# Optimization experiments

Hardware: AMD Instinct MI355X
Metric: run time of the kernel (lower is better)

The kernel has to match this reference:

```python
import jax, jax.numpy as jnp
import numpy as np

DIM = 512
NUM_HEADS = 8
POS_DIM = 2
K_CLUSTERS = 256
M_PTS = 256


def setup_inputs() -> dict:
    key = jax.random.key(0)
    ks = jax.random.split(key, 9)
    pos = jax.random.uniform(ks[0], (K_CLUSTERS, M_PTS, POS_DIM), dtype=jnp.float32)
    feat = jax.random.normal(ks[1], (K_CLUSTERS, M_PTS, DIM), dtype=jnp.float32)
    mask = jax.random.randint(ks[2], (K_CLUSTERS, M_PTS, 1), 0, 2, dtype=jnp.int32)
    s = 0.02
    qkv_w = jax.random.normal(ks[3], (DIM, 3 * DIM), dtype=jnp.float32) * s
    qkv_b = jnp.zeros((3 * DIM,), dtype=jnp.float32)
    pos_w = jax.random.normal(ks[4], (POS_DIM, NUM_HEADS), dtype=jnp.float32) * s
    pos_b = jnp.zeros((NUM_HEADS,), dtype=jnp.float32)
    proj_w = jax.random.normal(ks[5], (DIM, DIM), dtype=jnp.float32) * s
    proj_b = jnp.zeros((DIM,), dtype=jnp.float32)
    return {"pos": pos, "feat": feat, "qkv_w": qkv_w, "qkv_b": qkv_b,
            "pos_w": pos_w, "pos_b": pos_b, "proj_w": proj_w, "proj_b": proj_b,
            "mask": mask}


def reference(pos, feat, qkv_w, qkv_b, pos_w, pos_b, proj_w, proj_b, mask):
    k_, m, c = feat.shape
    H = pos_w.shape[1]
    hd = c // H
    scale = hd ** -0.5

    # qkv projection -> (3, k, H, m, hd)
    qkv = (feat @ qkv_w + qkv_b).reshape(k_, m, 3, H, hd).transpose(2, 0, 3, 1, 4)
    q, k, v = qkv[0], qkv[1], qkv[2]

    attn = jnp.einsum('khid,khjd->khij', q * scale, k)  # k,H,m,m

    # normalize each coordinate by its global max over all clusters/points
    pos_n = pos / jnp.max(pos, axis=(0, 1), keepdims=True)
    # rel_pos[k,a,b,d] = pos[k,b,d] - pos[k,a,d]
    rel_pos = pos_n[:, None, :, :] - pos_n[:, :, None, :]  # k,m,m,d
    pos_bias = rel_pos @ pos_w + pos_b                      # k,m,m,H
    attn = attn + pos_bias.transpose(0, 3, 1, 2)            # k,H,m,m

    # mask: k,m,1 -> additive bias over key dim
    maskf = mask[:, :, 0].astype(attn.dtype)                # k,m
    attn = attn + ((1.0 - maskf) * -100.0)[:, None, None, :]

    attn = jax.nn.softmax(attn, axis=-1)
    x = jnp.einsum('khij,khjd->khid', attn, v)              # k,H,m,hd
    x = x.transpose(0, 2, 1, 3).reshape(k_, m, c)
    x = x @ proj_w + proj_b
    return x
```

## Files before the change

kernel.cpp:

```cpp
#include <hip/hip_runtime.h>
#include <stdint.h>

typedef short bf16x8 __attribute__((ext_vector_type(8)));
typedef float f32x4 __attribute__((ext_vector_type(4)));
typedef unsigned short u16x4 __attribute__((ext_vector_type(4)));
typedef unsigned short ushort_t;

__device__ __forceinline__ float bf2f(unsigned short u) {
    union { unsigned int i; float f; } v; v.i = ((unsigned int)u) << 16; return v.f;
}
__device__ __forceinline__ unsigned short f2bf(float f) {
    union { float f; unsigned int i; } v; v.f = f;
    unsigned int r = (v.i + 0x7FFFu + ((v.i >> 16) & 1u)) >> 16;
    return (unsigned short)r;
}

__device__ __forceinline__ void gload_lds16(const void* g, void* l) {
    __builtin_amdgcn_global_load_lds(
        (const __attribute__((address_space(1))) void*)g,
        (__attribute__((address_space(3))) void*)l, 16, 0, 0);
}

template <bool F32> struct LD;
template <> struct LD<false> {
    static __device__ __forceinline__ float s(const void* p, size_t i) {
        return bf2f(((const ushort_t*)p)[i]);
    }
    static __device__ __forceinline__ bf16x8 v8(const void* p, size_t i) {
        return *reinterpret_cast<const bf16x8*>((const ushort_t*)p + i);
    }
};
template <> struct LD<true> {
    static __device__ __forceinline__ float s(const void* p, size_t i) {
        return ((const float*)p)[i];
    }
    static __device__ __forceinline__ bf16x8 v8(const void* p, size_t i) {
        const float* f = (const float*)p + i;
        float4 a = *reinterpret_cast<const float4*>(f);
        float4 b = *reinterpret_cast<const float4*>(f + 4);
        bf16x8 r;
        r[0] = (short)f2bf(a.x); r[1] = (short)f2bf(a.y);
        r[2] = (short)f2bf(a.z); r[3] = (short)f2bf(a.w);
        r[4] = (short)f2bf(b.x); r[5] = (short)f2bf(b.y);
        r[6] = (short)f2bf(b.z); r[7] = (short)f2bf(b.w);
        return r;
    }
};

__global__ __launch_bounds__(64) void kprobe(const ushort_t* __restrict__ pos, int* __restrict__ dt) {
    float v = bf2f(pos[2 * threadIdx.x]);
    bool sane = (v >= 0.0f) && (v <= 1.0f);
    unsigned long long b = __ballot(sane);
    if (threadIdx.x == 0) dt[0] = (b == ~0ULL) ? 1 : 0;
}

template <bool F32>
static __device__ __forceinline__ void kpos_body(const void* pos, int* pmax, float* s0, float* s1) {
    int p = blockIdx.x * 256 + threadIdx.x;
    s0[threadIdx.x] = LD<F32>::s(pos, 2 * (size_t)p);
    s1[threadIdx.x] = LD<F32>::s(pos, 2 * (size_t)p + 1);
    __syncthreads();
    for (int off = 128; off > 0; off >>= 1) {
        if (threadIdx.x < (unsigned)off) {
            s0[threadIdx.x] = fmaxf(s0[threadIdx.x], s0[threadIdx.x + off]);
            s1[threadIdx.x] = fmaxf(s1[threadIdx.x], s1[threadIdx.x + off]);
        }
        __syncthreads();
    }
    if (threadIdx.x == 0) {
        atomicMax(&pmax[0], __float_as_int(s0[0]));
        atomicMax(&pmax[1], __float_as_int(s1[0]));
    }
}
__global__ __launch_bounds__(256) void kpos_max(const int* __restrict__ dt, const void* __restrict__ pos,
                                                int* __restrict__ pmax) {
    __shared__ float s0[256], s1[256];
    if (dt[0]) kpos_body<false>(pos, pmax, s0, s1);
    else       kpos_body<true>(pos, pmax, s0, s1);
}

template <bool F32>
static __device__ __forceinline__ void ktb_body(const void* pos, const void* pos_w, const int* mask,
                                                const int* pmax, float* tb) {
    int p = blockIdx.x * 256 + threadIdx.x;
    float inv0 = 1.0f / __int_as_float(pmax[0]);
    float inv1 = 1.0f / __int_as_float(pmax[1]);
    float x0 = LD<F32>::s(pos, 2 * (size_t)p) * inv0;
    float x1 = LD<F32>::s(pos, 2 * (size_t)p + 1) * inv1;
    float mterm = mask[p] ? 0.0f : -100.0f;
#pragma unroll
    for (int h = 0; h < 8; h++)
        tb[p * 8 + h] = x0 * LD<F32>::s(pos_w, h) + x1 * LD<F32>::s(pos_w, 8 + h) + mterm;
}
__global__ __launch_bounds__(256) void ktb(const int* __restrict__ dt, const void* __restrict__ pos,
                                           const void* __restrict__ pos_w, const int* __restrict__ mask,
                                           const int* __restrict__ pmax, float* __restrict__ tb) {
    if (dt[0]) ktb_body<false>(pos, pos_w, mask, pmax, tb);
    else       ktb_body<true>(pos, pos_w, mask, pmax, tb);
}

__global__ __launch_bounds__(256) void kbias(const int* __restrict__ dt, const void* __restrict__ qkv_b,
                                             const void* __restrict__ proj_b,
                                             float* __restrict__ qb, float* __restrict__ pb) {
    int i = blockIdx.x * 256 + threadIdx.x;
    if (dt[0]) {
        if (i < 1536) qb[i] = bf2f(((const ushort_t*)qkv_b)[i]);
        if (i < 512)  pb[i] = bf2f(((const ushort_t*)proj_b)[i]);
    } else {
        if (i < 1536) qb[i] = ((const float*)qkv_b)[i];
        if (i < 512)  pb[i] = ((const float*)proj_b)[i];
    }
}

template <bool F32>
static __device__ __forceinline__ void kfeat_body(const void* feat, ushort_t* featb) {
    for (size_t t = (size_t)blockIdx.x * 256 + threadIdx.x; t < 4194304; t += (size_t)gridDim.x * 256) {
        *reinterpret_cast<bf16x8*>(featb + t * 8) = LD<F32>::v8(feat, t * 8);
    }
}
__global__ __launch_bounds__(256) void kfeat(const int* __restrict__ dt, const void* __restrict__ feat,
                                             ushort_t* __restrict__ featb) {
    if (dt[0]) kfeat_body<false>(feat, featb);
    else       kfeat_body<true>(feat, featb);
}

template <bool F32>
static __device__ __forceinline__ void ktrans_body(const void* src, ushort_t* dst, int R, int C,
                                                   ushort_t* tile ) {
    int nbc = C >> 6;
    int rb = (blockIdx.x / nbc) << 6;
    int cb = (blockIdx.x % nbc) << 6;
    for (int i = threadIdx.x; i < 4096; i += 256) {
        int r = i >> 6, c = i & 63;
        tile[r * 65 + c] = f2bf(LD<F32>::s(src, (size_t)(rb + r) * C + cb + c));
    }
    __syncthreads();
    for (int i = threadIdx.x; i < 4096; i += 256) {
        int rr = i & 63, cc = i >> 6;
        dst[(size_t)(cb + cc) * R + rb + rr] = tile[rr * 65 + cc];
    }
}
__global__ __launch_bounds__(256) void ktrans(const int* __restrict__ dt, const void* __restrict__ src,
                                              ushort_t* __restrict__ dst, int R, int C) {
    __shared__ ushort_t tile[64 * 65];
    if (dt[0]) ktrans_body<false>(src, dst, R, C, tile);
    else       ktrans_body<true>(src, dst, R, C, tile);
}

template <bool F32>
static __device__ __forceinline__ void kattn_body(const void* feat, const ushort_t* qkv_wt,
                                                  const float* qb, const float* tb, ushort_t* xout,
                                                  ushort_t* sQ, ushort_t* sK, ushort_t* sVt,
                                                  ushort_t* sP, float* stb) {
    const int tid = threadIdx.x;
    const int lane = tid & 63;
    const int wave = tid >> 6;
    const int quad = lane >> 4;
    const int l15 = lane & 15;

    const int bx = blockIdx.x;
    const int xcd = bx & 7;
    const int jj = bx >> 3;
    const int rr = jj >> 5;
    const int ss = jj & 31;
    const int kc = xcd * 32 + rr * 4 + (ss >> 3);
    const int h = ss & 7;

    if (tid < 256) stb[tid] = tb[(size_t)(kc * 256 + tid) * 8 + h];

    ushort_t* sW = sP;
    char* ldsW = (char*)sW;

    const int t1 = wave * 64 + lane;
    const int t2 = 512 + t1;
    const int lc1 = t1 >> 2, ch1 = t1 & 3;
    const int lc2 = t2 >> 2, ch2 = t2 & 3;
    const ushort_t* g1 = qkv_wt + (size_t)((lc1 >> 6) * 512 + h * 64 + (lc1 & 63)) * 512 + ch1 * 8;
    const ushort_t* g2 = qkv_wt + (size_t)((lc2 >> 6) * 512 + h * 64 + (lc2 & 63)) * 512 + ch2 * 8;

    const int wrow = (wave >> 1) * 64;
    const int wcol = (wave & 1) * 96;
    const int fcol = quad * 8;

    f32x4 acc[4][6];
#pragma unroll
    for (int rt = 0; rt < 4; rt++)
#pragma unroll
        for (int ct = 0; ct < 6; ct++) {
            f32x4 z = {0.0f, 0.0f, 0.0f, 0.0f};
            acc[rt][ct] = z;
        }

    const size_t fbase = (size_t)(kc * 256) * 512;

    gload_lds16(g1, ldsW + wave * 1024);
    if (wave < 4) gload_lds16(g2, ldsW + 8192 + wave * 1024);
    __syncthreads();

#pragma unroll 2
    for (int c = 0; c < 16; c++) {
        const int cb = (c & 1) * 6144;
        const int nbB = ((c + 1) & 1) * 12288;
        if (c < 15) {
            gload_lds16(g1 + (c + 1) * 32, ldsW + nbB + wave * 1024);
            if (wave < 4) gload_lds16(g2 + (c + 1) * 32, ldsW + nbB + 8192 + wave * 1024);
        }
        bf16x8 af[4];
#pragma unroll
        for (int rt = 0; rt < 4; rt++)
            af[rt] = LD<F32>::v8(feat, fbase + (size_t)(wrow + rt * 16 + l15) * 512 + c * 32 + fcol);
        bf16x8 bw[6];
#pragma unroll
        for (int ct = 0; ct < 6; ct++)
            bw[ct] = *reinterpret_cast<const bf16x8*>(sW + cb + (wcol + ct * 16 + l15) * 32 + fcol);
#pragma unroll
        for (int ct = 0; ct < 6; ct++)
#pragma unroll
            for (int rt = 0; rt < 4; rt++)
                acc[rt][ct] = __builtin_amdgcn_mfma_f32_16x16x32_bf16(af[rt], bw[ct], acc[rt][ct], 0, 0, 0);
        __syncthreads();
    }

#pragma unroll
    for (int ct = 0; ct < 6; ct++) {
        const int lcb = wcol + ct * 16;
        const int mat = lcb >> 6;
        const int col = (lcb & 63) + l15;
        const float bias = qb[mat * 512 + h * 64 + col];
#pragma unroll
        for (int rt = 0; rt < 4; rt++) {
            const int m0 = wrow + rt * 16 + quad * 4;
            if (mat == 0) {
#pragma unroll
                for (int r = 0; r < 4; r++)
                    sQ[(m0 + r) * 72 + col] = f2bf((acc[rt][ct][r] + bias) * 0.125f);
            } else if (mat == 1) {
#pragma unroll
                for (int r = 0; r < 4; r++)
                    sK[(m0 + r) * 72 + col] = f2bf(acc[rt][ct][r] + bias);
            } else {
                u16x4 vp;
#pragma unroll
                for (int r = 0; r < 4; r++) vp[r] = f2bf(acc[rt][ct][r] + bias);
                *reinterpret_cast<u16x4*>(&sVt[col * 264 + m0]) = vp;
            }
        }
    }
    __syncthreads();

    bf16x8 aQ[2][2];
#pragma unroll
    for (int rt = 0; rt < 2; rt++)
#pragma unroll
        for (int s = 0; s < 2; s++)
            aQ[rt][s] = *reinterpret_cast<const bf16x8*>(
                &sQ[(wave * 32 + rt * 16 + l15) * 72 + s * 32 + quad * 8]);

    f32x4 accO[2][4];
    float rs[2][4];
#pragma unroll
    for (int rt = 0; rt < 2; rt++)
#pragma unroll
        for (int ct = 0; ct < 4; ct++) {
            f32x4 z = {0.0f, 0.0f, 0.0f, 0.0f};
            accO[rt][ct] = z;
            rs[rt][ct] = 0.0f;
        }

    ushort_t* sPw = sP + wave * (32 * 72);

    for (int jb = 0; jb < 4; jb++) {
        int kb = jb * 64;
        bf16x8 bK[4][2];
#pragma unroll
        for (int ctk = 0; ctk < 4; ctk++)
#pragma unroll
            for (int s = 0; s < 2; s++)
                bK[ctk][s] = *reinterpret_cast<const bf16x8*>(
                    &sK[(kb + ctk * 16 + l15) * 72 + s * 32 + quad * 8]);

#pragma unroll
        for (int ctk = 0; ctk < 4; ctk++) {
            float tcol = stb[kb + ctk * 16 + l15];
#pragma unroll
            for (int rt = 0; rt < 2; rt++) {
                f32x4 sa = {0.0f, 0.0f, 0.0f, 0.0f};
                sa = __builtin_amdgcn_mfma_f32_16x16x32_bf16(aQ[rt][0], bK[ctk][0], sa, 0, 0, 0);
                sa = __builtin_amdgcn_mfma_f32_16x16x32_bf16(aQ[rt][1], bK[ctk][1], sa, 0, 0, 0);
                int rl0 = rt * 16 + quad * 4;
#pragma unroll
                for (int r = 0; r < 4; r++) {
                    float pexp = __expf(sa[r] + tcol);
                    rs[rt][r] += pexp;
                    sPw[(rl0 + r) * 72 + ctk * 16 + l15] = f2bf(pexp);
                }
            }
        }

#pragma unroll
        for (int s = 0; s < 2; s++) {
            bf16x8 aP[2];
#pragma unroll
            for (int rt = 0; rt < 2; rt++)
                aP[rt] = *reinterpret_cast<const bf16x8*>(
                    &sPw[(rt * 16 + l15) * 72 + s * 32 + quad * 8]);
#pragma unroll
            for (int ct = 0; ct < 4; ct++) {
                bf16x8 bV = *reinterpret_cast<const bf16x8*>(
                    &sVt[(ct * 16 + l15) * 264 + kb + s * 32 + quad * 8]);
#pragma unroll
                for (int rt = 0; rt < 2; rt++)
                    accO[rt][ct] =
                        __builtin_amdgcn_mfma_f32_16x16x32_bf16(aP[rt], bV, accO[rt][ct], 0, 0, 0);
            }
        }
    }

    float inv_[2][4];
#pragma unroll
    for (int rt = 0; rt < 2; rt++)
#pragma unroll
        for (int r = 0; r < 4; r++) {
            float v = rs[rt][r];
            v += __shfl_xor(v, 1, 64);
            v += __shfl_xor(v, 2, 64);
            v += __shfl_xor(v, 4, 64);
            v += __shfl_xor(v, 8, 64);
            inv_[rt][r] = 1.0f / v;
        }

#pragma unroll
    for (int rt = 0; rt < 2; rt++)
#pragma unroll
        for (int ct = 0; ct < 4; ct++)
#pragma unroll
            for (int r = 0; r < 4; r++) {
                int m = wave * 32 + rt * 16 + quad * 4 + r;
                xout[((size_t)(kc * 256 + m)) * 512 + h * 64 + ct * 16 + l15] =
                    f2bf(accO[rt][ct][r] * inv_[rt][r]);
            }
}
__global__ __launch_bounds__(512, 2) void kattn_bf(const ushort_t* __restrict__ featb,
                                                   const ushort_t* __restrict__ qkv_wt,
                                                   const float* __restrict__ qb,
                                                   const float* __restrict__ tb, ushort_t* __restrict__ xout) {
    __shared__ ushort_t sQ[256 * 72];
    __shared__ ushort_t sK[256 * 72];
    __shared__ ushort_t sVt[64 * 264];
    __shared__ ushort_t sP[8 * 32 * 72];
    __shared__ float stb[256];
    kattn_body<false>(featb, qkv_wt, qb, tb, xout, sQ, sK, sVt, sP, stb);
}
__global__ __launch_bounds__(512, 2) void kattn_dyn(const int* __restrict__ dt, const void* __restrict__ feat,
                                                    const ushort_t* __restrict__ qkv_wt,
                                                    const float* __restrict__ qb,
                                                    const float* __restrict__ tb, ushort_t* __restrict__ xout) {
    __shared__ ushort_t sQ[256 * 72];
    __shared__ ushort_t sK[256 * 72];
    __shared__ ushort_t sVt[64 * 264];
    __shared__ ushort_t sP[8 * 32 * 72];
    __shared__ float stb[256];
    if (dt[0]) kattn_body<false>(feat, qkv_wt, qb, tb, xout, sQ, sK, sVt, sP, stb);
    else       kattn_body<true>(feat, qkv_wt, qb, tb, xout, sQ, sK, sVt, sP, stb);
}

template <bool F32>
static __device__ __forceinline__ void kproj_body(const ushort_t* x, const ushort_t* proj_wt,
                                                  const float* pb, void* out, ushort_t* sW) {
    const int tid = threadIdx.x;
    const int lane = tid & 63;
    const int wave = tid >> 6;
    const int quad = lane >> 4;
    const int l15 = lane & 15;
    const int rowb = (blockIdx.x & 255) * 256 + wave * 64;
    const int colb = (blockIdx.x >> 8) * 128;
    char* ldsW = (char*)sW;

    const int t1 = wave * 64 + lane;
    const int t2 = t1 + 256;
    const ushort_t* g1 = proj_wt + (size_t)(colb + (t1 >> 2)) * 512 + (t1 & 3) * 8;
    const ushort_t* g2 = proj_wt + (size_t)(colb + (t2 >> 2)) * 512 + (t2 & 3) * 8;

    f32x4 acc[4][8];
#pragma unroll
    for (int rt = 0; rt < 4; rt++)
#pragma unroll
        for (int ct = 0; ct < 8; ct++) {
            f32x4 z = {0.0f, 0.0f, 0.0f, 0.0f};
            acc[rt][ct] = z;
        }

    gload_lds16(g1, ldsW + wave * 1024);
    gload_lds16(g2, ldsW + 4096 + wave * 1024);
    __syncthreads();

#pragma unroll 2
    for (int c = 0; c < 16; c++) {
        const int cb = (c & 1) * 4096;
        const int nbB = ((c + 1) & 1) * 8192;
        if (c < 15) {
            gload_lds16(g1 + (c + 1) * 32, ldsW + nbB + wave * 1024);
            gload_lds16(g2 + (c + 1) * 32, ldsW + nbB + 4096 + wave * 1024);
        }
        bf16x8 af[4];
#pragma unroll
        for (int rt = 0; rt < 4; rt++) {
            int m = rowb + rt * 16 + l15;
            af[rt] = *reinterpret_cast<const bf16x8*>(x + (size_t)m * 512 + c * 32 + quad * 8);
        }
        bf16x8 bw[8];
#pragma unroll
        for (int ct = 0; ct < 8; ct++)
            bw[ct] = *reinterpret_cast<const bf16x8*>(sW + cb + (ct * 16 + l15) * 32 + quad * 8);
#pragma unroll
        for (int ct = 0; ct < 8; ct++)
#pragma unroll
            for (int rt = 0; rt < 4; rt++)
                acc[rt][ct] = __builtin_amdgcn_mfma_f32_16x16x32_bf16(af[rt], bw[ct], acc[rt][ct], 0, 0, 0);
        __syncthreads();
    }

#pragma unroll
    for (int ct = 0; ct < 8; ct++) {
        int n = colb + ct * 16 + l15;
        float bias = pb[n];
#pragma unroll
        for (int rt = 0; rt < 4; rt++)
#pragma unroll
            for (int r = 0; r < 4; r++) {
                int m = rowb + rt * 16 + quad * 4 + r;
                float v = acc[rt][ct][r] + bias;
                if (F32) ((float*)out)[(size_t)m * 512 + n] = v;
                else     ((ushort_t*)out)[(size_t)m * 512 + n] = f2bf(v);
            }
    }
}
__global__ __launch_bounds__(256, 2) void kproj(const int* __restrict__ dt, const ushort_t* __restrict__ x,
                                                const ushort_t* __restrict__ proj_wt,
                                                const float* __restrict__ pb, void* __restrict__ out) {
    __shared__ ushort_t sW[2 * 128 * 32];
    if (dt[0]) kproj_body<false>(x, proj_wt, pb, out, sW);
    else       kproj_body<true>(x, proj_wt, pb, out, sW);
}

extern "C" void kernel_launch(void* const* d_in, const int* in_sizes, int n_in,
                              void* d_out, int out_size, void* d_ws, size_t ws_size,
                              hipStream_t stream) {
    (void)in_sizes; (void)n_in; (void)out_size;
    const void* pos    = d_in[0];
    const void* feat   = d_in[1];
    const void* qkv_w  = d_in[2];
    const void* qkv_b  = d_in[3];
    const void* pos_w  = d_in[4];
    const void* proj_w = d_in[6];
    const void* proj_b = d_in[7];
    const int* mask    = (const int*)d_in[8];

    char* ws = (char*)d_ws;
    int* pmax         = (int*)ws;
    int* dtf          = (int*)ws + 2;
    float* qb         = (float*)(ws + 256);
    float* pb         = (float*)(ws + 256 + 6144);
    float* tb         = (float*)(ws + 16384);
    ushort_t* qkv_wt  = (ushort_t*)(ws + 16384 + 2097152);
    ushort_t* proj_wt = qkv_wt + 786432;
    ushort_t* x       = proj_wt + 262144;
    ushort_t* featb   = x + 33554432;
    const size_t NEED = 16384 + 2097152 + 1572864 + 524288 + 67108864 + 67108864;
    const bool big = ws_size >= NEED;

    (void)hipMemsetAsync(ws, 0, 16, stream);
    kprobe<<<1, 64, 0, stream>>>((const ushort_t*)pos, dtf);
    kpos_max<<<256, 256, 0, stream>>>(dtf, pos, pmax);
    ktb<<<256, 256, 0, stream>>>(dtf, pos, pos_w, mask, pmax, tb);
    kbias<<<6, 256, 0, stream>>>(dtf, qkv_b, proj_b, qb, pb);
    ktrans<<<192, 256, 0, stream>>>(dtf, qkv_w, qkv_wt, 512, 1536);
    ktrans<<<64, 256, 0, stream>>>(dtf, proj_w, proj_wt, 512, 512);
    if (big) {
        kfeat<<<2048, 256, 0, stream>>>(dtf, feat, featb);
        kattn_bf<<<2048, 512, 0, stream>>>(featb, qkv_wt, qb, tb, x);
    } else {
        kattn_dyn<<<2048, 512, 0, stream>>>(dtf, feat, qkv_wt, qb, tb, x);
    }
    kproj<<<1024, 256, 0, stream>>>(dtf, x, proj_wt, pb, d_out);
}
```

Measured before the change: 582.1 us.

## Triple-buffer weight tiles with XOR swizzle and prefetch A fragments in GEMMs

Both the QKV stage of the attention kernel and the output projection kernel move from a double-buffered LDS weight pipeline with two __syncthreads per step to a three-stage ring buffer. Each step now needs only one s_barrier, uses manual vmcnt waits, and register-prefetches the next A fragment. LDS weight chunks are XOR-swizzled to cut bank conflicts on the bf16x8 reads. The projection kernel also narrows its column tile to 64 with XCD-aware block mapping and raises occupancy to 3 blocks, doubling the grid. The hand-counted vmcnt values and the single-barrier ring scheme are fragile: if the counts are wrong, it can read stale LDS data.

```diff
diff --git a/kernel.cpp b/kernel.cpp
--- a/kernel.cpp
+++ b/kernel.cpp
@@ -173,14 +173,14 @@
 
     const int t1 = wave * 64 + lane;
     const int t2 = 512 + t1;
-    const int lc1 = t1 >> 2, ch1 = t1 & 3;
-    const int lc2 = t2 >> 2, ch2 = t2 & 3;
+    const int lc1 = t1 >> 2, ch1 = (t1 & 3) ^ ((lc1 >> 1) & 3);
+    const int lc2 = t2 >> 2, ch2 = (t2 & 3) ^ ((lc2 >> 1) & 3);
     const ushort_t* g1 = qkv_wt + (size_t)((lc1 >> 6) * 512 + h * 64 + (lc1 & 63)) * 512 + ch1 * 8;
     const ushort_t* g2 = qkv_wt + (size_t)((lc2 >> 6) * 512 + h * 64 + (lc2 & 63)) * 512 + ch2 * 8;
 
     const int wrow = (wave >> 1) * 64;
     const int wcol = (wave & 1) * 96;
-    const int fcol = quad * 8;
+    const int swz = (l15 >> 1) & 3;
 
     f32x4 acc[4][6];
 #pragma unroll
@@ -192,33 +192,47 @@
         }
 
     const size_t fbase = (size_t)(kc * 256) * 512;
+    bf16x8 af[2][4];
 
     gload_lds16(g1, ldsW + wave * 1024);
     if (wave < 4) gload_lds16(g2, ldsW + 8192 + wave * 1024);
-    __syncthreads();
-
-#pragma unroll 2
+    gload_lds16(g1 + 32, ldsW + 12288 + wave * 1024);
+    if (wave < 4) gload_lds16(g2 + 32, ldsW + 12288 + 8192 + wave * 1024);
+    __builtin_amdgcn_sched_barrier(0);
+#pragma unroll
+    for (int rt = 0; rt < 4; rt++)
+        af[0][rt] = LD<F32>::v8(feat, fbase + (size_t)(wrow + rt * 16 + l15) * 512 + quad * 8);
+    if (F32) asm volatile("s_waitcnt vmcnt(9)" ::: "memory");
+    else     asm volatile("s_waitcnt vmcnt(5)" ::: "memory");
+    __builtin_amdgcn_sched_barrier(0);
+
+#pragma unroll
     for (int c = 0; c < 16; c++) {
-        const int cb = (c & 1) * 6144;
-        const int nbB = ((c + 1) & 1) * 12288;
-        if (c < 15) {
-            gload_lds16(g1 + (c + 1) * 32, ldsW + nbB + wave * 1024);
-            if (wave < 4) gload_lds16(g2 + (c + 1) * 32, ldsW + nbB + 8192 + wave * 1024);
-        }
-        bf16x8 af[4];
-#pragma unroll
-        for (int rt = 0; rt < 4; rt++)
-            af[rt] = LD<F32>::v8(feat, fbase + (size_t)(wrow + rt * 16 + l15) * 512 + c * 32 + fcol);
+        __builtin_amdgcn_s_barrier();
+        __builtin_amdgcn_sched_barrier(0);
+        if (c + 2 < 16) {
+            const int nb = ((c + 2) % 3) * 12288;
+            gload_lds16(g1 + (c + 2) * 32, ldsW + nb + wave * 1024);
+            if (wave < 4) gload_lds16(g2 + (c + 2) * 32, ldsW + nb + 8192 + wave * 1024);
+        }
+        __builtin_amdgcn_sched_barrier(0);
+        if (c + 1 < 16) {
+#pragma unroll
+            for (int rt = 0; rt < 4; rt++)
+                af[(c + 1) & 1][rt] = LD<F32>::v8(
+                    feat, fbase + (size_t)(wrow + rt * 16 + l15) * 512 + (c + 1) * 32 + quad * 8);
+        }
+        const int cbu = (c % 3) * 6144;
         bf16x8 bw[6];
 #pragma unroll
         for (int ct = 0; ct < 6; ct++)
-            bw[ct] = *reinterpret_cast<const bf16x8*>(sW + cb + (wcol + ct * 16 + l15) * 32 + fcol);
+            bw[ct] = *reinterpret_cast<const bf16x8*>(
+                sW + cbu + (wcol + ct * 16 + l15) * 32 + (quad ^ swz) * 8);
 #pragma unroll
         for (int ct = 0; ct < 6; ct++)
 #pragma unroll
             for (int rt = 0; rt < 4; rt++)
-                acc[rt][ct] = __builtin_amdgcn_mfma_f32_16x16x32_bf16(af[rt], bw[ct], acc[rt][ct], 0, 0, 0);
-        __syncthreads();
+                acc[rt][ct] = __builtin_amdgcn_mfma_f32_16x16x32_bf16(af[c & 1][rt], bw[ct], acc[rt][ct], 0, 0, 0);
     }
 
 #pragma unroll
@@ -372,73 +386,83 @@
     const int wave = tid >> 6;
     const int quad = lane >> 4;
     const int l15 = lane & 15;
-    const int rowb = (blockIdx.x & 255) * 256 + wave * 64;
-    const int colb = (blockIdx.x >> 8) * 128;
+    const int bx = blockIdx.x;
+    const int xcd = bx & 7;
+    const int j = bx >> 3;
+    const int rowb = (xcd * 32 + (j >> 3)) * 256;
+    const int colb = (j & 7) * 64;
     char* ldsW = (char*)sW;
 
-    const int t1 = wave * 64 + lane;
-    const int t2 = t1 + 256;
-    const ushort_t* g1 = proj_wt + (size_t)(colb + (t1 >> 2)) * 512 + (t1 & 3) * 8;
-    const ushort_t* g2 = proj_wt + (size_t)(colb + (t2 >> 2)) * 512 + (t2 & 3) * 8;
-
-    f32x4 acc[4][8];
+    const int lc = tid >> 2, ch = (tid & 3) ^ ((lc >> 1) & 3);
+    const ushort_t* g1 = proj_wt + (size_t)(colb + lc) * 512 + ch * 8;
+    const int swz = (l15 >> 1) & 3;
+
+    f32x4 acc[4][4];
 #pragma unroll
     for (int rt = 0; rt < 4; rt++)
 #pragma unroll
-        for (int ct = 0; ct < 8; ct++) {
+        for (int ct = 0; ct < 4; ct++) {
             f32x4 z = {0.0f, 0.0f, 0.0f, 0.0f};
             acc[rt][ct] = z;
         }
 
+    bf16x8 af[2][4];
+
     gload_lds16(g1, ldsW + wave * 1024);
-    gload_lds16(g2, ldsW + 4096 + wave * 1024);
-    __syncthreads();
-
-#pragma unroll 2
+    gload_lds16(g1 + 32, ldsW + 4096 + wave * 1024);
+    __builtin_amdgcn_sched_barrier(0);
+#pragma unroll
+    for (int rt = 0; rt < 4; rt++)
+        af[0][rt] = *reinterpret_cast<const bf16x8*>(
+            x + (size_t)(rowb + wave * 64 + rt * 16 + l15) * 512 + quad * 8);
+    asm volatile("s_waitcnt vmcnt(5)" ::: "memory");
+    __builtin_amdgcn_sched_barrier(0);
+
+#pragma unroll
     for (int c = 0; c < 16; c++) {
-        const int cb = (c & 1) * 4096;
-        const int nbB = ((c + 1) & 1) * 8192;
-        if (c < 15) {
-            gload_lds16(g1 + (c + 1) * 32, ldsW + nbB + wave * 1024);
-            gload_lds16(g2 + (c + 1) * 32, ldsW + nbB + 4096 + wave * 1024);
-        }
-        bf16x8 af[4];
-#pragma unroll
-        for (int rt = 0; rt < 4; rt++) {
-            int m = rowb + rt * 16 + l15;
-            af[rt] = *reinterpret_cast<const bf16x8*>(x + (size_t)m * 512 + c * 32 + quad * 8);
-        }
-        bf16x8 bw[8];
-#pragma unroll
-        for (int ct = 0; ct < 8; ct++)
-            bw[ct] = *reinterpret_cast<const bf16x8*>(sW + cb + (ct * 16 + l15) * 32 + quad * 8);
-#pragma unroll
-        for (int ct = 0; ct < 8; ct++)
+        __builtin_amdgcn_s_barrier();
+        __builtin_amdgcn_sched_barrier(0);
+        if (c + 2 < 16)
+            gload_lds16(g1 + (c + 2) * 32, ldsW + ((c + 2) % 3) * 4096 + wave * 1024);
+        __builtin_amdgcn_sched_barrier(0);
+        if (c + 1 < 16) {
 #pragma unroll
             for (int rt = 0; rt < 4; rt++)
-                acc[rt][ct] = __builtin_amdgcn_mfma_f32_16x16x32_bf16(af[rt], bw[ct], acc[rt][ct], 0, 0, 0);
-        __syncthreads();
-    }
-
-#pragma unroll
-    for (int ct = 0; ct < 8; ct++) {
+                af[(c + 1) & 1][rt] = *reinterpret_cast<const bf16x8*>(
+                    x + (size_t)(rowb + wave * 64 + rt * 16 + l15) * 512 + (c + 1) * 32 + quad * 8);
+        }
+        const int cbu = (c % 3) * 2048;
+        bf16x8 bw[4];
+#pragma unroll
+        for (int ct = 0; ct < 4; ct++)
+            bw[ct] = *reinterpret_cast<const bf16x8*>(
+                sW + cbu + (ct * 16 + l15) * 32 + (quad ^ swz) * 8);
+#pragma unroll
+        for (int ct = 0; ct < 4; ct++)
+#pragma unroll
+            for (int rt = 0; rt < 4; rt++)
+                acc[rt][ct] = __builtin_amdgcn_mfma_f32_16x16x32_bf16(af[c & 1][rt], bw[ct], acc[rt][ct], 0, 0, 0);
+    }
+
+#pragma unroll
+    for (int ct = 0; ct < 4; ct++) {
         int n = colb + ct * 16 + l15;
         float bias = pb[n];
 #pragma unroll
         for (int rt = 0; rt < 4; rt++)
 #pragma unroll
             for (int r = 0; r < 4; r++) {
-                int m = rowb + rt * 16 + quad * 4 + r;
+                int m = rowb + wave * 64 + rt * 16 + quad * 4 + r;
                 float v = acc[rt][ct][r] + bias;
                 if (F32) ((float*)out)[(size_t)m * 512 + n] = v;
                 else     ((ushort_t*)out)[(size_t)m * 512 + n] = f2bf(v);
             }
     }
 }
-__global__ __launch_bounds__(256, 2) void kproj(const int* __restrict__ dt, const ushort_t* __restrict__ x,
+__global__ __launch_bounds__(256, 3) void kproj(const int* __restrict__ dt, const ushort_t* __restrict__ x,
                                                 const ushort_t* __restrict__ proj_wt,
                                                 const float* __restrict__ pb, void* __restrict__ out) {
-    __shared__ ushort_t sW[2 * 128 * 32];
+    __shared__ ushort_t sW[3 * 64 * 32];
     if (dt[0]) kproj_body<false>(x, proj_wt, pb, out, sW);
     else       kproj_body<true>(x, proj_wt, pb, out, sW);
 }
@@ -482,5 +506,5 @@
     } else {
         kattn_dyn<<<2048, 512, 0, stream>>>(dtf, feat, qkv_wt, qb, tb, x);
     }
-    kproj<<<1024, 256, 0, stream>>>(dtf, x, proj_wt, pb, d_out);
-}
+    kproj<<<2048, 256, 0, stream>>>(dtf, x, proj_wt, pb, d_out);
+}
```

Measured after the change: 584.8 us. No clear change (+0.5%).

## Double wave count per block in attention and projection kernels, swizzle LDS weights

Applied to the files above, without the earlier changes.

The attention kernel now launches 1024 threads (16 waves), so each wave owns a 64x48 QKV tile and 16 query rows instead of a 64x96 tile and 32 rows. The projection kernel now uses 512 threads with 64x64 tiles per wave and an XCD-aware block remap. Both stage their weights with an XOR swizzle on the 16-byte chunk index to cut LDS bank conflicts. The aim is more waves in flight and lower register pressure per wave to hide latency. The cost is more redundant global feat/x fragment loads per block and heavier barrier synchronisation.

```diff
diff --git a/kernel.cpp b/kernel.cpp
--- a/kernel.cpp
+++ b/kernel.cpp
@@ -171,50 +171,44 @@
     ushort_t* sW = sP;
     char* ldsW = (char*)sW;
 
-    const int t1 = wave * 64 + lane;
-    const int t2 = 512 + t1;
-    const int lc1 = t1 >> 2, ch1 = t1 & 3;
-    const int lc2 = t2 >> 2, ch2 = t2 & 3;
+    const int lc1 = tid >> 2, ch1 = (tid & 3) ^ ((lc1 >> 1) & 3);
     const ushort_t* g1 = qkv_wt + (size_t)((lc1 >> 6) * 512 + h * 64 + (lc1 & 63)) * 512 + ch1 * 8;
-    const ushort_t* g2 = qkv_wt + (size_t)((lc2 >> 6) * 512 + h * 64 + (lc2 & 63)) * 512 + ch2 * 8;
-
-    const int wrow = (wave >> 1) * 64;
-    const int wcol = (wave & 1) * 96;
-    const int fcol = quad * 8;
-
-    f32x4 acc[4][6];
+    const bool stager = (tid < 768);
+
+    const int wrow = (wave >> 2) * 64;
+    const int wcol = (wave & 3) * 48;
+    const int swz = (l15 >> 1) & 3;
+
+    f32x4 acc[4][3];
 #pragma unroll
     for (int rt = 0; rt < 4; rt++)
 #pragma unroll
-        for (int ct = 0; ct < 6; ct++) {
+        for (int ct = 0; ct < 3; ct++) {
             f32x4 z = {0.0f, 0.0f, 0.0f, 0.0f};
             acc[rt][ct] = z;
         }
 
     const size_t fbase = (size_t)(kc * 256) * 512;
 
-    gload_lds16(g1, ldsW + wave * 1024);
-    if (wave < 4) gload_lds16(g2, ldsW + 8192 + wave * 1024);
+    if (stager) gload_lds16(g1, ldsW + wave * 1024);
     __syncthreads();
 
 #pragma unroll 2
     for (int c = 0; c < 16; c++) {
         const int cb = (c & 1) * 6144;
-        const int nbB = ((c + 1) & 1) * 12288;
-        if (c < 15) {
-            gload_lds16(g1 + (c + 1) * 32, ldsW + nbB + wave * 1024);
-            if (wave < 4) gload_lds16(g2 + (c + 1) * 32, ldsW + nbB + 8192 + wave * 1024);
-        }
+        if (c < 15 && stager)
+            gload_lds16(g1 + (c + 1) * 32, ldsW + ((c + 1) & 1) * 12288 + wave * 1024);
         bf16x8 af[4];
 #pragma unroll
         for (int rt = 0; rt < 4; rt++)
-            af[rt] = LD<F32>::v8(feat, fbase + (size_t)(wrow + rt * 16 + l15) * 512 + c * 32 + fcol);
-        bf16x8 bw[6];
-#pragma unroll
-        for (int ct = 0; ct < 6; ct++)
-            bw[ct] = *reinterpret_cast<const bf16x8*>(sW + cb + (wcol + ct * 16 + l15) * 32 + fcol);
-#pragma unroll
-        for (int ct = 0; ct < 6; ct++)
+            af[rt] = LD<F32>::v8(feat, fbase + (size_t)(wrow + rt * 16 + l15) * 512 + c * 32 + quad * 8);
+        bf16x8 bw[3];
+#pragma unroll
+        for (int ct = 0; ct < 3; ct++)
+            bw[ct] = *reinterpret_cast<const bf16x8*>(
+                sW + cb + (wcol + ct * 16 + l15) * 32 + (quad ^ swz) * 8);
+#pragma unroll
+        for (int ct = 0; ct < 3; ct++)
 #pragma unroll
             for (int rt = 0; rt < 4; rt++)
                 acc[rt][ct] = __builtin_amdgcn_mfma_f32_16x16x32_bf16(af[rt], bw[ct], acc[rt][ct], 0, 0, 0);
@@ -222,7 +216,7 @@
     }
 
 #pragma unroll
-    for (int ct = 0; ct < 6; ct++) {
+    for (int ct = 0; ct < 3; ct++) {
         const int lcb = wcol + ct * 16;
         const int mat = lcb >> 6;
         const int col = (lcb & 63) + l15;
@@ -248,26 +242,22 @@
     }
     __syncthreads();
 
-    bf16x8 aQ[2][2];
-#pragma unroll
-    for (int rt = 0; rt < 2; rt++)
-#pragma unroll
-        for (int s = 0; s < 2; s++)
-            aQ[rt][s] = *reinterpret_cast<const bf16x8*>(
-                &sQ[(wave * 32 + rt * 16 + l15) * 72 + s * 32 + quad * 8]);
-
-    f32x4 accO[2][4];
-    float rs[2][4];
-#pragma unroll
-    for (int rt = 0; rt < 2; rt++)
-#pragma unroll
-        for (int ct = 0; ct < 4; ct++) {
-            f32x4 z = {0.0f, 0.0f, 0.0f, 0.0f};
-            accO[rt][ct] = z;
-            rs[rt][ct] = 0.0f;
-        }
-
-    ushort_t* sPw = sP + wave * (32 * 72);
+    bf16x8 aQ[2];
+#pragma unroll
+    for (int s = 0; s < 2; s++)
+        aQ[s] = *reinterpret_cast<const bf16x8*>(
+            &sQ[(wave * 16 + l15) * 72 + s * 32 + quad * 8]);
+
+    f32x4 accO[4];
+    float rs[4];
+#pragma unroll
+    for (int ct = 0; ct < 4; ct++) {
+        f32x4 z = {0.0f, 0.0f, 0.0f, 0.0f};
+        accO[ct] = z;
+        rs[ct] = 0.0f;
+    }
+
+    ushort_t* sPw = sP + wave * (16 * 72);
 
     for (int jb = 0; jb < 4; jb++) {
         int kb = jb * 64;
@@ -282,83 +272,70 @@
 #pragma unroll
         for (int ctk = 0; ctk < 4; ctk++) {
             float tcol = stb[kb + ctk * 16 + l15];
-#pragma unroll
-            for (int rt = 0; rt < 2; rt++) {
-                f32x4 sa = {0.0f, 0.0f, 0.0f, 0.0f};
-                sa = __builtin_amdgcn_mfma_f32_16x16x32_bf16(aQ[rt][0], bK[ctk][0], sa, 0, 0, 0);
-                sa = __builtin_amdgcn_mfma_f32_16x16x32_bf16(aQ[rt][1], bK[ctk][1], sa, 0, 0, 0);
-                int rl0 = rt * 16 + quad * 4;
-#pragma unroll
-                for (int r = 0; r < 4; r++) {
-                    float pexp = __expf(sa[r] + tcol);
-                    rs[rt][r] += pexp;
-                    sPw[(rl0 + r) * 72 + ctk * 16 + l15] = f2bf(pexp);
-                }
+            f32x4 sa = {0.0f, 0.0f, 0.0f, 0.0f};
+            sa = __builtin_amdgcn_mfma_f32_16x16x32_bf16(aQ[0], bK[ctk][0], sa, 0, 0, 0);
+            sa = __builtin_amdgcn_mfma_f32_16x16x32_bf16(aQ[1], bK[ctk][1], sa, 0, 0, 0);
+            int rl0 = quad * 4;
+#pragma unroll
+            for (int r = 0; r < 4; r++) {
+                float pexp = __expf(sa[r] + tcol);
+                rs[r] += pexp;
+                sPw[(rl0 + r) * 72 + ctk * 16 + l15] = f2bf(pexp);
             }
         }
 
 #pragma unroll
         for (int s = 0; s < 2; s++) {
-            bf16x8 aP[2];
-#pragma unroll
-            for (int rt = 0; rt < 2; rt++)
-                aP[rt] = *reinterpret_cast<const bf16x8*>(
-                    &sPw[(rt * 16 + l15) * 72 + s * 32 + quad * 8]);
+            bf16x8 aP = *reinterpret_cast<const bf16x8*>(
+                &sPw[l15 * 72 + s * 32 + quad * 8]);
 #pragma unroll
             for (int ct = 0; ct < 4; ct++) {
                 bf16x8 bV = *reinterpret_cast<const bf16x8*>(
                     &sVt[(ct * 16 + l15) * 264 + kb + s * 32 + quad * 8]);
-#pragma unroll
-                for (int rt = 0; rt < 2; rt++)
-                    accO[rt][ct] =
-                        __builtin_amdgcn_mfma_f32_16x16x32_bf16(aP[rt], bV, accO[rt][ct], 0, 0, 0);
+                accO[ct] = __builtin_amdgcn_mfma_f32_16x16x32_bf16(aP, bV, accO[ct], 0, 0, 0);
             }
         }
     }
 
-    float inv_[2][4];
-#pragma unroll
-    for (int rt = 0; rt < 2; rt++)
+    float inv_[4];
+#pragma unroll
+    for (int r = 0; r < 4; r++) {
+        float v = rs[r];
+        v += __shfl_xor(v, 1, 64);
+        v += __shfl_xor(v, 2, 64);
+        v += __shfl_xor(v, 4, 64);
+        v += __shfl_xor(v, 8, 64);
+        inv_[r] = 1.0f / v;
+    }
+
+#pragma unroll
+    for (int ct = 0; ct < 4; ct++)
 #pragma unroll
         for (int r = 0; r < 4; r++) {
-            float v = rs[rt][r];
-            v += __shfl_xor(v, 1, 64);
-            v += __shfl_xor(v, 2, 64);
-            v += __shfl_xor(v, 4, 64);
-            v += __shfl_xor(v, 8, 64);
-            inv_[rt][r] = 1.0f / v;
-        }
-
-#pragma unroll
-    for (int rt = 0; rt < 2; rt++)
-#pragma unroll
-        for (int ct = 0; ct < 4; ct++)
-#pragma unroll
-            for (int r = 0; r < 4; r++) {
-                int m = wave * 32 + rt * 16 + quad * 4 + r;
-                xout[((size_t)(kc * 256 + m)) * 512 + h * 64 + ct * 16 + l15] =
-                    f2bf(accO[rt][ct][r] * inv_[rt][r]);
-            }
-}
-__global__ __launch_bounds__(512, 2) void kattn_bf(const ushort_t* __restrict__ featb,
-                                                   const ushort_t* __restrict__ qkv_wt,
-                                                   const float* __restrict__ qb,
-                                                   const float* __restrict__ tb, ushort_t* __restrict__ xout) {
-    __shared__ ushort_t sQ[256 * 72];
-    __shared__ ushort_t sK[256 * 72];
-    __shared__ ushort_t sVt[64 * 264];
-    __shared__ ushort_t sP[8 * 32 * 72];
-    __shared__ float stb[256];
-    kattn_body<false>(featb, qkv_wt, qb, tb, xout, sQ, sK, sVt, sP, stb);
-}
-__global__ __launch_bounds__(512, 2) void kattn_dyn(const int* __restrict__ dt, const void* __restrict__ feat,
+            int m = wave * 16 + quad * 4 + r;
+            xout[((size_t)(kc * 256 + m)) * 512 + h * 64 + ct * 16 + l15] =
+                f2bf(accO[ct][r] * inv_[r]);
+        }
+}
+__global__ __launch_bounds__(1024, 4) void kattn_bf(const ushort_t* __restrict__ featb,
                                                     const ushort_t* __restrict__ qkv_wt,
                                                     const float* __restrict__ qb,
                                                     const float* __restrict__ tb, ushort_t* __restrict__ xout) {
     __shared__ ushort_t sQ[256 * 72];
     __shared__ ushort_t sK[256 * 72];
     __shared__ ushort_t sVt[64 * 264];
-    __shared__ ushort_t sP[8 * 32 * 72];
+    __shared__ ushort_t sP[16 * 16 * 72];
+    __shared__ float stb[256];
+    kattn_body<false>(featb, qkv_wt, qb, tb, xout, sQ, sK, sVt, sP, stb);
+}
+__global__ __launch_bounds__(1024, 4) void kattn_dyn(const int* __restrict__ dt, const void* __restrict__ feat,
+                                                     const ushort_t* __restrict__ qkv_wt,
+                                                     const float* __restrict__ qb,
+                                                     const float* __restrict__ tb, ushort_t* __restrict__ xout) {
+    __shared__ ushort_t sQ[256 * 72];
+    __shared__ ushort_t sK[256 * 72];
+    __shared__ ushort_t sVt[64 * 264];
+    __shared__ ushort_t sP[16 * 16 * 72];
     __shared__ float stb[256];
     if (dt[0]) kattn_body<false>(feat, qkv_wt, qb, tb, xout, sQ, sK, sVt, sP, stb);
     else       kattn_body<true>(feat, qkv_wt, qb, tb, xout, sQ, sK, sVt, sP, stb);
@@ -372,48 +349,49 @@
     const int wave = tid >> 6;
     const int quad = lane >> 4;
     const int l15 = lane & 15;
-    const int rowb = (blockIdx.x & 255) * 256 + wave * 64;
-    const int colb = (blockIdx.x >> 8) * 128;
+    const int bx = blockIdx.x;
+    const int xcd = bx & 7;
+    const int j = bx >> 3;
+    const int rowb = (xcd * 32 + (j >> 2)) * 256;
+    const int colb = (j & 3) * 128;
+    const int rowg = (wave >> 1) * 64;
+    const int colg = (wave & 1) * 64;
     char* ldsW = (char*)sW;
 
-    const int t1 = wave * 64 + lane;
-    const int t2 = t1 + 256;
-    const ushort_t* g1 = proj_wt + (size_t)(colb + (t1 >> 2)) * 512 + (t1 & 3) * 8;
-    const ushort_t* g2 = proj_wt + (size_t)(colb + (t2 >> 2)) * 512 + (t2 & 3) * 8;
-
-    f32x4 acc[4][8];
+    const int lc = tid >> 2, ch = (tid & 3) ^ ((lc >> 1) & 3);
+    const ushort_t* g1 = proj_wt + (size_t)(colb + lc) * 512 + ch * 8;
+    const int swz = (l15 >> 1) & 3;
+
+    f32x4 acc[4][4];
 #pragma unroll
     for (int rt = 0; rt < 4; rt++)
 #pragma unroll
-        for (int ct = 0; ct < 8; ct++) {
+        for (int ct = 0; ct < 4; ct++) {
             f32x4 z = {0.0f, 0.0f, 0.0f, 0.0f};
             acc[rt][ct] = z;
         }
 
     gload_lds16(g1, ldsW + wave * 1024);
-    gload_lds16(g2, ldsW + 4096 + wave * 1024);
     __syncthreads();
 
 #pragma unroll 2
     for (int c = 0; c < 16; c++) {
         const int cb = (c & 1) * 4096;
-        const int nbB = ((c + 1) & 1) * 8192;
-        if (c < 15) {
-            gload_lds16(g1 + (c + 1) * 32, ldsW + nbB + wave * 1024);
-            gload_lds16(g2 + (c + 1) * 32, ldsW + nbB + 4096 + wave * 1024);
-        }
+        if (c < 15)
+            gload_lds16(g1 + (c + 1) * 32, ldsW + ((c + 1) & 1) * 8192 + wave * 1024);
         bf16x8 af[4];
 #pragma unroll
         for (int rt = 0; rt < 4; rt++) {
-            int m = rowb + rt * 16 + l15;
+            int m = rowb + rowg + rt * 16 + l15;
             af[rt] = *reinterpret_cast<const bf16x8*>(x + (size_t)m * 512 + c * 32 + quad * 8);
         }
-        bf16x8 bw[8];
-#pragma unroll
-        for (int ct = 0; ct < 8; ct++)
-            bw[ct] = *reinterpret_cast<const bf16x8*>(sW + cb + (ct * 16 + l15) * 32 + quad * 8);
-#pragma unroll
-        for (int ct = 0; ct < 8; ct++)
+        bf16x8 bw[4];
+#pragma unroll
+        for (int ct = 0; ct < 4; ct++)
+            bw[ct] = *reinterpret_cast<const bf16x8*>(
+                sW + cb + (colg + ct * 16 + l15) * 32 + (quad ^ swz) * 8);
+#pragma unroll
+        for (int ct = 0; ct < 4; ct++)
 #pragma unroll
             for (int rt = 0; rt < 4; rt++)
                 acc[rt][ct] = __builtin_amdgcn_mfma_f32_16x16x32_bf16(af[rt], bw[ct], acc[rt][ct], 0, 0, 0);
@@ -421,21 +399,21 @@
     }
 
 #pragma unroll
-    for (int ct = 0; ct < 8; ct++) {
-        int n = colb + ct * 16 + l15;
+    for (int ct = 0; ct < 4; ct++) {
+        int n = colb + colg + ct * 16 + l15;
         float bias = pb[n];
 #pragma unroll
         for (int rt = 0; rt < 4; rt++)
 #pragma unroll
             for (int r = 0; r < 4; r++) {
-                int m = rowb + rt * 16 + quad * 4 + r;
+                int m = rowb + rowg + rt * 16 + quad * 4 + r;
                 float v = acc[rt][ct][r] + bias;
                 if (F32) ((float*)out)[(size_t)m * 512 + n] = v;
                 else     ((ushort_t*)out)[(size_t)m * 512 + n] = f2bf(v);
             }
     }
 }
-__global__ __launch_bounds__(256, 2) void kproj(const int* __restrict__ dt, const ushort_t* __restrict__ x,
+__global__ __launch_bounds__(512, 4) void kproj(const int* __restrict__ dt, const ushort_t* __restrict__ x,
                                                 const ushort_t* __restrict__ proj_wt,
                                                 const float* __restrict__ pb, void* __restrict__ out) {
     __shared__ ushort_t sW[2 * 128 * 32];
@@ -478,9 +456,9 @@
     ktrans<<<64, 256, 0, stream>>>(dtf, proj_w, proj_wt, 512, 512);
     if (big) {
         kfeat<<<2048, 256, 0, stream>>>(dtf, feat, featb);
-        kattn_bf<<<2048, 512, 0, stream>>>(featb, qkv_wt, qb, tb, x);
+        kattn_bf<<<2048, 1024, 0, stream>>>(featb, qkv_wt, qb, tb, x);
     } else {
-        kattn_dyn<<<2048, 512, 0, stream>>>(dtf, feat, qkv_wt, qb, tb, x);
-    }
-    kproj<<<1024, 256, 0, stream>>>(dtf, x, proj_wt, pb, d_out);
-}
+        kattn_dyn<<<2048, 1024, 0, stream>>>(dtf, feat, qkv_wt, qb, tb, x);
+    }
+    kproj<<<1024, 512, 0, stream>>>(dtf, x, proj_wt, pb, d_out);
+}
```

Result: slower. 658.8 us (+13.2%).

## Double K-step with XOR-swizzled LDS weight staging in attention and projection GEMMs

Applied to the files above, without the earlier changes.

Weight tiles for both GEMMs are now staged 64 columns of K per iteration instead of 32, halving the number of barriers and refill rounds. An XOR swizzle on the 16-byte chunk index is applied to the LDS layout to avoid bank conflicts on reads. The projection kernel moves to 512 threads with a 2x2 wave grid and an XCD-aware block remap so that neighbouring column blocks share rows of x in cache. The attention kernel's shared memory is merged into one array so the larger staging buffer can overlay the Q/K regions, which adds aliasing risk between phases.

```diff
diff --git a/kernel.cpp b/kernel.cpp
--- a/kernel.cpp
+++ b/kernel.cpp
@@ -150,8 +150,7 @@
 template <bool F32>
 static __device__ __forceinline__ void kattn_body(const void* feat, const ushort_t* qkv_wt,
                                                   const float* qb, const float* tb, ushort_t* xout,
-                                                  ushort_t* sQ, ushort_t* sK, ushort_t* sVt,
-                                                  ushort_t* sP, float* stb) {
+                                                  ushort_t* smem) {
     const int tid = threadIdx.x;
     const int lane = tid & 63;
     const int wave = tid >> 6;
@@ -166,21 +165,23 @@
     const int kc = xcd * 32 + rr * 4 + (ss >> 3);
     const int h = ss & 7;
 
+    ushort_t* sQ  = smem;
+    ushort_t* sK  = smem + 18432;
+    ushort_t* sVt = smem + 36864;
+    ushort_t* sP  = smem + 53760;
+    float*    stb = (float*)(smem + 72192);
+    char*     stg = (char*)smem;
+
     if (tid < 256) stb[tid] = tb[(size_t)(kc * 256 + tid) * 8 + h];
 
-    ushort_t* sW = sP;
-    char* ldsW = (char*)sW;
-
-    const int t1 = wave * 64 + lane;
-    const int t2 = 512 + t1;
-    const int lc1 = t1 >> 2, ch1 = t1 & 3;
-    const int lc2 = t2 >> 2, ch2 = t2 & 3;
-    const ushort_t* g1 = qkv_wt + (size_t)((lc1 >> 6) * 512 + h * 64 + (lc1 & 63)) * 512 + ch1 * 8;
-    const ushort_t* g2 = qkv_wt + (size_t)((lc2 >> 6) * 512 + h * 64 + (lc2 & 63)) * 512 + ch2 * 8;
+    const int t0 = tid, t1 = tid + 512, t2 = tid + 1024;
+    const int r0 = t0 >> 3, r1 = t1 >> 3, r2 = t2 >> 3;
+    const ushort_t* g0 = qkv_wt + (size_t)((r0 >> 6) * 512 + h * 64 + (r0 & 63)) * 512 + (((t0 & 7) ^ (r0 & 7)) * 8);
+    const ushort_t* g1 = qkv_wt + (size_t)((r1 >> 6) * 512 + h * 64 + (r1 & 63)) * 512 + (((t1 & 7) ^ (r1 & 7)) * 8);
+    const ushort_t* g2 = qkv_wt + (size_t)((r2 >> 6) * 512 + h * 64 + (r2 & 63)) * 512 + (((t2 & 7) ^ (r2 & 7)) * 8);
 
     const int wrow = (wave >> 1) * 64;
     const int wcol = (wave & 1) * 96;
-    const int fcol = quad * 8;
 
     f32x4 acc[4][6];
 #pragma unroll
@@ -193,31 +194,40 @@
 
     const size_t fbase = (size_t)(kc * 256) * 512;
 
-    gload_lds16(g1, ldsW + wave * 1024);
-    if (wave < 4) gload_lds16(g2, ldsW + 8192 + wave * 1024);
+    gload_lds16(g0, stg + t0 * 16);
+    gload_lds16(g1, stg + t1 * 16);
+    gload_lds16(g2, stg + t2 * 16);
     __syncthreads();
 
 #pragma unroll 2
-    for (int c = 0; c < 16; c++) {
-        const int cb = (c & 1) * 6144;
-        const int nbB = ((c + 1) & 1) * 12288;
-        if (c < 15) {
-            gload_lds16(g1 + (c + 1) * 32, ldsW + nbB + wave * 1024);
-            if (wave < 4) gload_lds16(g2 + (c + 1) * 32, ldsW + nbB + 8192 + wave * 1024);
-        }
-        bf16x8 af[4];
-#pragma unroll
-        for (int rt = 0; rt < 4; rt++)
-            af[rt] = LD<F32>::v8(feat, fbase + (size_t)(wrow + rt * 16 + l15) * 512 + c * 32 + fcol);
-        bf16x8 bw[6];
-#pragma unroll
-        for (int ct = 0; ct < 6; ct++)
-            bw[ct] = *reinterpret_cast<const bf16x8*>(sW + cb + (wcol + ct * 16 + l15) * 32 + fcol);
-#pragma unroll
-        for (int ct = 0; ct < 6; ct++)
+    for (int it = 0; it < 8; it++) {
+        if (it < 7) {
+            const int nb = ((it + 1) & 1) * 24576;
+            gload_lds16(g0 + (it + 1) * 64, stg + nb + t0 * 16);
+            gload_lds16(g1 + (it + 1) * 64, stg + nb + t1 * 16);
+            gload_lds16(g2 + (it + 1) * 64, stg + nb + t2 * 16);
+        }
+        const int cbu = (it & 1) * 12288;
+#pragma unroll
+        for (int s = 0; s < 2; s++) {
+            bf16x8 af[4];
 #pragma unroll
             for (int rt = 0; rt < 4; rt++)
-                acc[rt][ct] = __builtin_amdgcn_mfma_f32_16x16x32_bf16(af[rt], bw[ct], acc[rt][ct], 0, 0, 0);
+                af[rt] = LD<F32>::v8(
+                    feat, fbase + (size_t)(wrow + rt * 16 + l15) * 512 + it * 64 + s * 32 + quad * 8);
+            bf16x8 bw[6];
+#pragma unroll
+            for (int ct = 0; ct < 6; ct++) {
+                const int rw = wcol + ct * 16 + l15;
+                bw[ct] = *reinterpret_cast<const bf16x8*>(
+                    smem + cbu + rw * 64 + (((s * 4 + quad) ^ (rw & 7)) * 8));
+            }
+#pragma unroll
+            for (int ct = 0; ct < 6; ct++)
+#pragma unroll
+                for (int rt = 0; rt < 4; rt++)
+                    acc[rt][ct] = __builtin_amdgcn_mfma_f32_16x16x32_bf16(af[rt], bw[ct], acc[rt][ct], 0, 0, 0);
+        }
         __syncthreads();
     }
 
@@ -344,24 +354,16 @@
                                                    const ushort_t* __restrict__ qkv_wt,
                                                    const float* __restrict__ qb,
                                                    const float* __restrict__ tb, ushort_t* __restrict__ xout) {
-    __shared__ ushort_t sQ[256 * 72];
-    __shared__ ushort_t sK[256 * 72];
-    __shared__ ushort_t sVt[64 * 264];
-    __shared__ ushort_t sP[8 * 32 * 72];
-    __shared__ float stb[256];
-    kattn_body<false>(featb, qkv_wt, qb, tb, xout, sQ, sK, sVt, sP, stb);
+    __shared__ ushort_t smem[72704];
+    kattn_body<false>(featb, qkv_wt, qb, tb, xout, smem);
 }
 __global__ __launch_bounds__(512, 2) void kattn_dyn(const int* __restrict__ dt, const void* __restrict__ feat,
                                                     const ushort_t* __restrict__ qkv_wt,
                                                     const float* __restrict__ qb,
                                                     const float* __restrict__ tb, ushort_t* __restrict__ xout) {
-    __shared__ ushort_t sQ[256 * 72];
-    __shared__ ushort_t sK[256 * 72];
-    __shared__ ushort_t sVt[64 * 264];
-    __shared__ ushort_t sP[8 * 32 * 72];
-    __shared__ float stb[256];
-    if (dt[0]) kattn_body<false>(feat, qkv_wt, qb, tb, xout, sQ, sK, sVt, sP, stb);
-    else       kattn_body<true>(feat, qkv_wt, qb, tb, xout, sQ, sK, sVt, sP, stb);
+    __shared__ ushort_t smem[72704];
+    if (dt[0]) kattn_body<false>(feat, qkv_wt, qb, tb, xout, smem);
+    else       kattn_body<true>(feat, qkv_wt, qb, tb, xout, smem);
 }
 
 template <bool F32>
@@ -372,73 +374,85 @@
     const int wave = tid >> 6;
     const int quad = lane >> 4;
     const int l15 = lane & 15;
-    const int rowb = (blockIdx.x & 255) * 256 + wave * 64;
-    const int colb = (blockIdx.x >> 8) * 128;
-    char* ldsW = (char*)sW;
-
-    const int t1 = wave * 64 + lane;
-    const int t2 = t1 + 256;
-    const ushort_t* g1 = proj_wt + (size_t)(colb + (t1 >> 2)) * 512 + (t1 & 3) * 8;
-    const ushort_t* g2 = proj_wt + (size_t)(colb + (t2 >> 2)) * 512 + (t2 & 3) * 8;
-
-    f32x4 acc[4][8];
+    const int bx = blockIdx.x;
+    const int xcd = bx & 7;
+    const int j = bx >> 3;
+    const int rowb = (xcd * 32 + (j >> 2)) * 256;
+    const int colb = (j & 3) * 128;
+    const int rowg = (wave >> 1) * 64;
+    const int colg = (wave & 1) * 64;
+    char* stg = (char*)sW;
+
+    const int t0 = tid, t1 = tid + 512;
+    const int r0 = t0 >> 3, r1 = t1 >> 3;
+    const ushort_t* g0 = proj_wt + (size_t)(colb + r0) * 512 + (((t0 & 7) ^ (r0 & 7)) * 8);
+    const ushort_t* g1 = proj_wt + (size_t)(colb + r1) * 512 + (((t1 & 7) ^ (r1 & 7)) * 8);
+
+    f32x4 acc[4][4];
 #pragma unroll
     for (int rt = 0; rt < 4; rt++)
 #pragma unroll
-        for (int ct = 0; ct < 8; ct++) {
+        for (int ct = 0; ct < 4; ct++) {
             f32x4 z = {0.0f, 0.0f, 0.0f, 0.0f};
             acc[rt][ct] = z;
         }
 
-    gload_lds16(g1, ldsW + wave * 1024);
-    gload_lds16(g2, ldsW + 4096 + wave * 1024);
+    gload_lds16(g0, stg + t0 * 16);
+    gload_lds16(g1, stg + t1 * 16);
     __syncthreads();
 
 #pragma unroll 2
-    for (int c = 0; c < 16; c++) {
-        const int cb = (c & 1) * 4096;
-        const int nbB = ((c + 1) & 1) * 8192;
-        if (c < 15) {
-            gload_lds16(g1 + (c + 1) * 32, ldsW + nbB + wave * 1024);
-            gload_lds16(g2 + (c + 1) * 32, ldsW + nbB + 4096 + wave * 1024);
-        }
-        bf16x8 af[4];
-#pragma unroll
-        for (int rt = 0; rt < 4; rt++) {
-            int m = rowb + rt * 16 + l15;
-            af[rt] = *reinterpret_cast<const bf16x8*>(x + (size_t)m * 512 + c * 32 + quad * 8);
-        }
-        bf16x8 bw[8];
-#pragma unroll
-        for (int ct = 0; ct < 8; ct++)
-            bw[ct] = *reinterpret_cast<const bf16x8*>(sW + cb + (ct * 16 + l15) * 32 + quad * 8);
-#pragma unroll
-        for (int ct = 0; ct < 8; ct++)
-#pragma unroll
-            for (int rt = 0; rt < 4; rt++)
-                acc[rt][ct] = __builtin_amdgcn_mfma_f32_16x16x32_bf16(af[rt], bw[ct], acc[rt][ct], 0, 0, 0);
+    for (int it = 0; it < 8; it++) {
+        if (it < 7) {
+            const int nb = ((it + 1) & 1) * 16384;
+            gload_lds16(g0 + (it + 1) * 64, stg + nb + t0 * 16);
+            gload_lds16(g1 + (it + 1) * 64, stg + nb + t1 * 16);
+        }
+        const int cbu = (it & 1) * 8192;
+#pragma unroll
+        for (int s = 0; s < 2; s++) {
+            bf16x8 af[4];
+#pragma unroll
+            for (int rt = 0; rt < 4; rt++) {
+                int m = rowb + rowg + rt * 16 + l15;
+                af[rt] = *reinterpret_cast<const bf16x8*>(
+                    x + (size_t)m * 512 + it * 64 + s * 32 + quad * 8);
+            }
+            bf16x8 bw[4];
+#pragma unroll
+            for (int ct = 0; ct < 4; ct++) {
+                const int rw = colg + ct * 16 + l15;
+                bw[ct] = *reinterpret_cast<const bf16x8*>(
+                    sW + cbu + rw * 64 + (((s * 4 + quad) ^ (rw & 7)) * 8));
+            }
+#pragma unroll
+            for (int ct = 0; ct < 4; ct++)
+#pragma unroll
+                for (int rt = 0; rt < 4; rt++)
+                    acc[rt][ct] = __builtin_amdgcn_mfma_f32_16x16x32_bf16(af[rt], bw[ct], acc[rt][ct], 0, 0, 0);
+        }
         __syncthreads();
     }
 
 #pragma unroll
-    for (int ct = 0; ct < 8; ct++) {
-        int n = colb + ct * 16 + l15;
+    for (int ct = 0; ct < 4; ct++) {
+        int n = colb + colg + ct * 16 + l15;
         float bias = pb[n];
 #pragma unroll
         for (int rt = 0; rt < 4; rt++)
 #pragma unroll
             for (int r = 0; r < 4; r++) {
-                int m = rowb + rt * 16 + quad * 4 + r;
+                int m = rowb + rowg + rt * 16 + quad * 4 + r;
                 float v = acc[rt][ct][r] + bias;
                 if (F32) ((float*)out)[(size_t)m * 512 + n] = v;
                 else     ((ushort_t*)out)[(size_t)m * 512 + n] = f2bf(v);
             }
     }
 }
-__global__ __launch_bounds__(256, 2) void kproj(const int* __restrict__ dt, const ushort_t* __restrict__ x,
+__global__ __launch_bounds__(512, 4) void kproj(const int* __restrict__ dt, const ushort_t* __restrict__ x,
                                                 const ushort_t* __restrict__ proj_wt,
                                                 const float* __restrict__ pb, void* __restrict__ out) {
-    __shared__ ushort_t sW[2 * 128 * 32];
+    __shared__ ushort_t sW[16384];
     if (dt[0]) kproj_body<false>(x, proj_wt, pb, out, sW);
     else       kproj_body<true>(x, proj_wt, pb, out, sW);
 }
@@ -482,5 +496,5 @@
     } else {
         kattn_dyn<<<2048, 512, 0, stream>>>(dtf, feat, qkv_wt, qb, tb, x);
     }
-    kproj<<<1024, 256, 0, stream>>>(dtf, x, proj_wt, pb, d_out);
-}
+    kproj<<<1024, 512, 0, stream>>>(dtf, x, proj_wt, pb, d_out);
+}
```

After: 594.3 us. 2.1% more time.
